# Optimization experiments

Measured on AMD Instinct MI355X. Metric: run time of the kernel, lower is better.

## Reference

```python
import jax, jax.numpy as jnp
import numpy as np

DIM = 384
FRACTION = 16   # quant_bits=16 -> fixed-point fraction bits
INTEGER = 16
WEIGHT_BITS = 5
SHIFT_MIN = -(2 ** (WEIGHT_BITS - 1) - 2)  # -14 (DeepShift shift_range for 5-bit)


def _ste(x, qx):
    # straight-through estimator: forward qx, backward identity
    return x + jax.lax.stop_gradient(qx - x)


def _clampabs(w, mn, mx):
    # clamp |w| into [mn, mx], preserving sign (zeros stay zero)
    return jnp.sign(w) * jnp.clip(jnp.abs(w), mn, mx)


def _round_power_of_2(w):
    # w -> sign(w) * 2^round(log2(|w|))
    shift = jnp.round(jnp.log2(jnp.maximum(jnp.abs(w), 1e-30)))
    return jnp.sign(w) * jnp.exp2(shift)


def _round_to_fixed(x, fraction=FRACTION, integer=INTEGER):
    delta = 2.0 ** (-fraction)
    bound = 2.0 ** (integer - 1)
    return jnp.clip(jnp.floor(x / delta) * delta, -bound, bound - 1)


def setup_inputs() -> dict:
    key = jax.random.key(0)
    k1, k2, k3 = jax.random.split(key, 3)
    x = jax.random.normal(k1, (32, DIM, 56, 56), dtype=jnp.float32)
    weight = jax.random.normal(k2, (DIM, 1, 3, 3), dtype=jnp.float32) * 0.1
    bias = jax.random.normal(k3, (DIM,), dtype=jnp.float32) * 0.01
    return {"x": x, "weight": weight, "bias": bias}


def reference(x, weight, bias):
    # weight: clamp magnitude to [2^-14, 2^0], then round to signed power of two (5-bit shift)
    w = _ste(weight, _clampabs(weight, 2.0 ** SHIFT_MIN, 1.0))
    w = _ste(w, _round_power_of_2(w))
    # activations / bias: 16-bit fixed-point rounding
    xq = _ste(x, _round_to_fixed(x))
    bq = _ste(bias, _round_to_fixed(bias))
    # depthwise 3x3 conv, stride 1, padding 1, groups = DIM
    out = jax.lax.conv_general_dilated(
        xq, w,
        window_strides=(1, 1),
        padding=((1, 1), (1, 1)),
        feature_group_count=DIM,
        dimension_numbers=("NCHW", "OIHW", "NCHW"),
    )
    return out + bq[None, :, None, None]
```

## Files before the change

kernel.cpp:

```cpp
#include <hip/hip_runtime.h>


#define DW_C   384
#define DW_H   56
#define DW_W   56
#define DW_HW  (DW_H * DW_W)
#define DW_HW4 (DW_HW / 4)
#define DW_W4  (DW_W / 4)

__device__ __forceinline__ float qfix(float v) {
    v = floorf(v * 65536.0f) * (1.0f / 65536.0f);
    return fminf(fmaxf(v, -32768.0f), 32767.0f);
}

__global__ __launch_bounds__(256) void peg_shift_dwconv(
    const float* __restrict__ x, const float* __restrict__ wgt,
    const float* __restrict__ bias, float* __restrict__ out)
{
    __shared__ float s[DW_HW];

    const int plane = blockIdx.x;
    const int c = plane % DW_C;
    const float* xp = x + (size_t)plane * DW_HW;
    float* op = out + (size_t)plane * DW_HW;

    const float4* xp4 = (const float4*)xp;
    float4* s4 = (float4*)s;
    for (int i = threadIdx.x; i < DW_HW4; i += 256) {
        float4 v = xp4[i];
        v.x = qfix(v.x); v.y = qfix(v.y); v.z = qfix(v.z); v.w = qfix(v.w);
        s4[i] = v;
    }

    float wq[9];
#pragma unroll
    for (int k = 0; k < 9; ++k) {
        float wv = wgt[c * 9 + k];
        float aw = fabsf(wv);
        float cw = fminf(fmaxf(aw, 6.103515625e-05f ), 1.0f);
        float q  = exp2f(rintf(log2f(cw)));
        wq[k] = (wv > 0.0f) ? q : ((wv < 0.0f) ? -q : 0.0f);
    }
    float bq = qfix(bias[c]);

    __syncthreads();

    for (int iv = threadIdx.x; iv < DW_HW4; iv += 256) {
        int h  = iv / DW_W4;
        int w0 = (iv - h * DW_W4) * 4;
        float a0 = bq, a1 = bq, a2 = bq, a3 = bq;
#pragma unroll
        for (int dh = 0; dh < 3; ++dh) {
            int hh = h + dh - 1;
            if (hh < 0 || hh >= DW_H) continue;
            const float* row = s + hh * DW_W;
            float4 m = *(const float4*)(row + w0);
            float left  = (w0 > 0)        ? row[w0 - 1] : 0.0f;
            float right = (w0 < DW_W - 4) ? row[w0 + 4] : 0.0f;
            float wl = wq[dh * 3 + 0], wm = wq[dh * 3 + 1], wr = wq[dh * 3 + 2];
            a0 += left * wl + m.x * wm + m.y * wr;
            a1 += m.x  * wl + m.y * wm + m.z * wr;
            a2 += m.y  * wl + m.z * wm + m.w * wr;
            a3 += m.z  * wl + m.w * wm + right * wr;
        }
        float4 o; o.x = a0; o.y = a1; o.z = a2; o.w = a3;
        ((float4*)op)[iv] = o;
    }
}

extern "C" void kernel_launch(void* const* d_in, const int* in_sizes, int n_in,
                              void* d_out, int out_size, void* d_ws, size_t ws_size,
                              hipStream_t stream) {
    const float* x = (const float*)d_in[0];
    const float* w = (const float*)d_in[1];
    const float* b = (const float*)d_in[2];
    float* out = (float*)d_out;

    int planes = in_sizes[0] / DW_HW;
    peg_shift_dwconv<<<planes, 256, 0, stream>>>(x, w, b, out);
}
```

Measured before the change: 269.6 us.

## Replace LDS plane staging with register rolling row window and lane shuffles

Each 16-lane group now handles half of one channel plane. Each lane owns a 4-wide column strip and walks 28 rows down the plane, keeping three quantized rows in registers and prefetching the next raw row. Horizontal halo values come from wavefront shuffles instead of shared memory, which removes the LDS fill, the block barrier and the repeated LDS reads. The cost is 2 of every 16 lanes idling (56 columns only need 14 strips) and extra halo row loads at the split between the two halves.

```diff
diff --git a/kernel.cpp b/kernel.cpp
--- a/kernel.cpp
+++ b/kernel.cpp
@@ -5,66 +5,89 @@
 #define DW_H   56
 #define DW_W   56
 #define DW_HW  (DW_H * DW_W)
-#define DW_HW4 (DW_HW / 4)
-#define DW_W4  (DW_W / 4)
+#define HALF_H 28
 
 __device__ __forceinline__ float qfix(float v) {
     v = floorf(v * 65536.0f) * (1.0f / 65536.0f);
     return fminf(fmaxf(v, -32768.0f), 32767.0f);
 }
 
+struct QRow { float l; float4 m; float r; };
+
 __global__ __launch_bounds__(256) void peg_shift_dwconv(
     const float* __restrict__ x, const float* __restrict__ wgt,
     const float* __restrict__ bias, float* __restrict__ out)
 {
-    __shared__ float s[DW_HW];
-
-    const int plane = blockIdx.x;
-    const int c = plane % DW_C;
-    const float* xp = x + (size_t)plane * DW_HW;
-    float* op = out + (size_t)plane * DW_HW;
-
-    const float4* xp4 = (const float4*)xp;
-    float4* s4 = (float4*)s;
-    for (int i = threadIdx.x; i < DW_HW4; i += 256) {
-        float4 v = xp4[i];
-        v.x = qfix(v.x); v.y = qfix(v.y); v.z = qfix(v.z); v.w = qfix(v.w);
-        s4[i] = v;
-    }
+    const int lane16 = threadIdx.x & 15;
+    const int g      = threadIdx.x >> 4;
+    const int unit   = blockIdx.x * 16 + g;
+    const int plane  = unit >> 1;
+    const int half   = unit & 1;
+    const int c      = plane % DW_C;
+    const int strip  = lane16;
+    const bool active = strip < 14;
+    const int w0     = strip * 4;
 
     float wq[9];
 #pragma unroll
     for (int k = 0; k < 9; ++k) {
         float wv = wgt[c * 9 + k];
-        float aw = fabsf(wv);
-        float cw = fminf(fmaxf(aw, 6.103515625e-05f ), 1.0f);
+        float cw = fminf(fmaxf(fabsf(wv), 6.103515625e-05f ), 1.0f);
         float q  = exp2f(rintf(log2f(cw)));
         wq[k] = (wv > 0.0f) ? q : ((wv < 0.0f) ? -q : 0.0f);
     }
-    float bq = qfix(bias[c]);
+    const float bq = qfix(bias[c]);
 
-    __syncthreads();
+    const float* xp = x   + (size_t)plane * DW_HW + w0;
+    float*       op = out + (size_t)plane * DW_HW + w0;
+    const int h0 = half * HALF_H;
 
-    for (int iv = threadIdx.x; iv < DW_HW4; iv += 256) {
-        int h  = iv / DW_W4;
-        int w0 = (iv - h * DW_W4) * 4;
+    auto load_row = [&](int r) -> float4 {
+        if (active && r >= 0 && r < DW_H)
+            return *(const float4*)(xp + r * DW_W);
+        return make_float4(0.f, 0.f, 0.f, 0.f);
+    };
+
+    auto process = [&](float4 raw) -> QRow {
+        QRow t;
+        t.m.x = qfix(raw.x); t.m.y = qfix(raw.y);
+        t.m.z = qfix(raw.z); t.m.w = qfix(raw.w);
+        float up = __shfl_up(t.m.w, 1, 64);
+        float dn = __shfl_down(t.m.x, 1, 64);
+        t.l = (strip > 0)  ? up : 0.f;
+        t.r = (strip < 13) ? dn : 0.f;
+        return t;
+    };
+
+    float4 ra   = load_row(h0 - 1);
+    float4 rb   = load_row(h0);
+    float4 rawc = load_row(h0 + 1);
+    QRow qm1 = process(ra);
+    QRow q0  = process(rb);
+
+    for (int i = 0; i < HALF_H; ++i) {
+        float4 rawn = load_row(h0 + i + 2);
+        QRow q1 = process(rawc);
+
         float a0 = bq, a1 = bq, a2 = bq, a3 = bq;
-#pragma unroll
-        for (int dh = 0; dh < 3; ++dh) {
-            int hh = h + dh - 1;
-            if (hh < 0 || hh >= DW_H) continue;
-            const float* row = s + hh * DW_W;
-            float4 m = *(const float4*)(row + w0);
-            float left  = (w0 > 0)        ? row[w0 - 1] : 0.0f;
-            float right = (w0 < DW_W - 4) ? row[w0 + 4] : 0.0f;
-            float wl = wq[dh * 3 + 0], wm = wq[dh * 3 + 1], wr = wq[dh * 3 + 2];
-            a0 += left * wl + m.x * wm + m.y * wr;
-            a1 += m.x  * wl + m.y * wm + m.z * wr;
-            a2 += m.y  * wl + m.z * wm + m.w * wr;
-            a3 += m.z  * wl + m.w * wm + right * wr;
+        a0 += qm1.l   * wq[0] + qm1.m.x * wq[1] + qm1.m.y * wq[2];
+        a1 += qm1.m.x * wq[0] + qm1.m.y * wq[1] + qm1.m.z * wq[2];
+        a2 += qm1.m.y * wq[0] + qm1.m.z * wq[1] + qm1.m.w * wq[2];
+        a3 += qm1.m.z * wq[0] + qm1.m.w * wq[1] + qm1.r   * wq[2];
+        a0 += q0.l   * wq[3] + q0.m.x * wq[4] + q0.m.y * wq[5];
+        a1 += q0.m.x * wq[3] + q0.m.y * wq[4] + q0.m.z * wq[5];
+        a2 += q0.m.y * wq[3] + q0.m.z * wq[4] + q0.m.w * wq[5];
+        a3 += q0.m.z * wq[3] + q0.m.w * wq[4] + q0.r   * wq[5];
+        a0 += q1.l   * wq[6] + q1.m.x * wq[7] + q1.m.y * wq[8];
+        a1 += q1.m.x * wq[6] + q1.m.y * wq[7] + q1.m.z * wq[8];
+        a2 += q1.m.y * wq[6] + q1.m.z * wq[7] + q1.m.w * wq[8];
+        a3 += q1.m.z * wq[6] + q1.m.w * wq[7] + q1.r   * wq[8];
+
+        if (active) {
+            float4 o; o.x = a0; o.y = a1; o.z = a2; o.w = a3;
+            *(float4*)(op + (h0 + i) * DW_W) = o;
         }
-        float4 o; o.x = a0; o.y = a1; o.z = a2; o.w = a3;
-        ((float4*)op)[iv] = o;
+        qm1 = q0; q0 = q1; rawc = rawn;
     }
 }
 
@@ -77,5 +100,6 @@
     float* out = (float*)d_out;
 
     int planes = in_sizes[0] / DW_HW;
-    peg_shift_dwconv<<<planes, 256, 0, stream>>>(x, w, b, out);
+    int blocks = planes * 2 / 16;
+    peg_shift_dwconv<<<blocks, 256, 0, stream>>>(x, w, b, out);
 }
```

After: 291.1 us. +8.0%, slower.

## Replace LDS staging with per-wave register streaming and shuffle-based halo exchange

Applied to the files above, without the earlier changes.

Each wavefront now handles one whole plane. Lanes are laid out as 4 row-groups by 16 column-vectors, and the plane is streamed in 14 groups of 4 rows with the next loads prefetched into registers. Horizontal and vertical halos move through cross-lane shuffles instead of shared memory, which removes the LDS stage and the block barrier. In exchange it adds many shuffles per output, leaves 2 of every 16 lanes idle, and launches a quarter as many blocks.

```diff
diff --git a/kernel.cpp b/kernel.cpp
--- a/kernel.cpp
+++ b/kernel.cpp
@@ -1,70 +1,119 @@
 #include <hip/hip_runtime.h>
 
 
-#define DW_C   384
-#define DW_H   56
-#define DW_W   56
-#define DW_HW  (DW_H * DW_W)
-#define DW_HW4 (DW_HW / 4)
-#define DW_W4  (DW_W / 4)
+#define DW_C    384
+#define DW_H    56
+#define DW_W    56
+#define DW_HW   (DW_H * DW_W)
+#define NGRP    14
 
 __device__ __forceinline__ float qfix(float v) {
     v = floorf(v * 65536.0f) * (1.0f / 65536.0f);
     return fminf(fmaxf(v, -32768.0f), 32767.0f);
 }
 
+struct P3 { float4 U, M, D; };
+
+__device__ __forceinline__ float4 shfl_up4(float4 v, int d) {
+    float4 r;
+    r.x = __shfl_up(v.x, d, 64); r.y = __shfl_up(v.y, d, 64);
+    r.z = __shfl_up(v.z, d, 64); r.w = __shfl_up(v.w, d, 64);
+    return r;
+}
+__device__ __forceinline__ float4 shfl_dn4(float4 v, int d) {
+    float4 r;
+    r.x = __shfl_down(v.x, d, 64); r.y = __shfl_down(v.y, d, 64);
+    r.z = __shfl_down(v.z, d, 64); r.w = __shfl_down(v.w, d, 64);
+    return r;
+}
+
 __global__ __launch_bounds__(256) void peg_shift_dwconv(
     const float* __restrict__ x, const float* __restrict__ wgt,
     const float* __restrict__ bias, float* __restrict__ out)
 {
-    __shared__ float s[DW_HW];
-
-    const int plane = blockIdx.x;
-    const int c = plane % DW_C;
-    const float* xp = x + (size_t)plane * DW_HW;
-    float* op = out + (size_t)plane * DW_HW;
-
-    const float4* xp4 = (const float4*)xp;
-    float4* s4 = (float4*)s;
-    for (int i = threadIdx.x; i < DW_HW4; i += 256) {
-        float4 v = xp4[i];
-        v.x = qfix(v.x); v.y = qfix(v.y); v.z = qfix(v.z); v.w = qfix(v.w);
-        s4[i] = v;
-    }
+    const int lane  = threadIdx.x & 63;
+    const int wave  = threadIdx.x >> 6;
+    const int plane = blockIdx.x * 4 + wave;
+    const int rg    = lane >> 4;
+    const int w4    = lane & 15;
+    const bool active = w4 < 14;
+    const int c     = plane % DW_C;
 
     float wq[9];
 #pragma unroll
     for (int k = 0; k < 9; ++k) {
         float wv = wgt[c * 9 + k];
-        float aw = fabsf(wv);
-        float cw = fminf(fmaxf(aw, 6.103515625e-05f ), 1.0f);
+        float cw = fminf(fmaxf(fabsf(wv), 6.103515625e-05f ), 1.0f);
         float q  = exp2f(rintf(log2f(cw)));
         wq[k] = (wv > 0.0f) ? q : ((wv < 0.0f) ? -q : 0.0f);
     }
-    float bq = qfix(bias[c]);
+    const float bq = qfix(bias[c]);
 
-    __syncthreads();
+    const int   lane_off = rg * DW_W + w4 * 4;
+    const float* xp = x   + (size_t)plane * DW_HW + lane_off;
+    float*       op = out + (size_t)plane * DW_HW + lane_off;
 
-    for (int iv = threadIdx.x; iv < DW_HW4; iv += 256) {
-        int h  = iv / DW_W4;
-        int w0 = (iv - h * DW_W4) * 4;
-        float a0 = bq, a1 = bq, a2 = bq, a3 = bq;
-#pragma unroll
-        for (int dh = 0; dh < 3; ++dh) {
-            int hh = h + dh - 1;
-            if (hh < 0 || hh >= DW_H) continue;
-            const float* row = s + hh * DW_W;
-            float4 m = *(const float4*)(row + w0);
-            float left  = (w0 > 0)        ? row[w0 - 1] : 0.0f;
-            float right = (w0 < DW_W - 4) ? row[w0 + 4] : 0.0f;
-            float wl = wq[dh * 3 + 0], wm = wq[dh * 3 + 1], wr = wq[dh * 3 + 2];
-            a0 += left * wl + m.x * wm + m.y * wr;
-            a1 += m.x  * wl + m.y * wm + m.z * wr;
-            a2 += m.y  * wl + m.z * wm + m.w * wr;
-            a3 += m.z  * wl + m.w * wm + right * wr;
+    auto load_grp = [&](int g) -> float4 {
+        if (active) return *(const float4*)(xp + g * (4 * DW_W));
+        return make_float4(0.f, 0.f, 0.f, 0.f);
+    };
+
+    auto partials = [&](float4 raw) -> P3 {
+        float4 m;
+        m.x = qfix(raw.x); m.y = qfix(raw.y);
+        m.z = qfix(raw.z); m.w = qfix(raw.w);
+        float l = __shfl_up(m.w, 1, 64);   l = (w4 > 0)  ? l : 0.f;
+        float r = __shfl_down(m.x, 1, 64); r = (w4 < 13) ? r : 0.f;
+        P3 p;
+        p.U.x = l*wq[0] + m.x*wq[1] + m.y*wq[2];
+        p.U.y = m.x*wq[0] + m.y*wq[1] + m.z*wq[2];
+        p.U.z = m.y*wq[0] + m.z*wq[1] + m.w*wq[2];
+        p.U.w = m.z*wq[0] + m.w*wq[1] + r*wq[2];
+        p.M.x = bq + l*wq[3] + m.x*wq[4] + m.y*wq[5];
+        p.M.y = bq + m.x*wq[3] + m.y*wq[4] + m.z*wq[5];
+        p.M.z = bq + m.y*wq[3] + m.z*wq[4] + m.w*wq[5];
+        p.M.w = bq + m.z*wq[3] + m.w*wq[4] + r*wq[5];
+        p.D.x = l*wq[6] + m.x*wq[7] + m.y*wq[8];
+        p.D.y = m.x*wq[6] + m.y*wq[7] + m.z*wq[8];
+        p.D.z = m.y*wq[6] + m.z*wq[7] + m.w*wq[8];
+        p.D.w = m.z*wq[6] + m.w*wq[7] + r*wq[8];
+        return p;
+    };
+
+    float4 raw0 = load_grp(0);
+    float4 rawN = load_grp(1);
+    P3 P0 = partials(raw0);
+    float4 carryU = make_float4(0.f, 0.f, 0.f, 0.f);
+    const float4 zero4 = make_float4(0.f, 0.f, 0.f, 0.f);
+
+    for (int i = 0; i < NGRP; ++i) {
+        float4 raw2 = (i + 2 < NGRP) ? load_grp(i + 2) : zero4;
+
+        P3 P1;
+        if (i + 1 < NGRP) P1 = partials(rawN);
+        else              { P1.U = zero4; P1.M = zero4; P1.D = zero4; }
+
+        float4 dn_cross = shfl_up4(P1.D, 48);
+        float4 upS = shfl_up4(P0.U, 16);
+        float4 dnS = shfl_dn4(P0.D, 16);
+        float4 up, dn;
+        up.x = (rg > 0) ? upS.x : carryU.x;  up.y = (rg > 0) ? upS.y : carryU.y;
+        up.z = (rg > 0) ? upS.z : carryU.z;  up.w = (rg > 0) ? upS.w : carryU.w;
+        dn.x = (rg < 3) ? dnS.x : dn_cross.x; dn.y = (rg < 3) ? dnS.y : dn_cross.y;
+        dn.z = (rg < 3) ? dnS.z : dn_cross.z; dn.w = (rg < 3) ? dnS.w : dn_cross.w;
+
+        if (active) {
+            float4 o;
+            o.x = up.x + P0.M.x + dn.x;
+            o.y = up.y + P0.M.y + dn.y;
+            o.z = up.z + P0.M.z + dn.z;
+            o.w = up.w + P0.M.w + dn.w;
+            *(float4*)(op + i * (4 * DW_W)) = o;
         }
-        float4 o; o.x = a0; o.y = a1; o.z = a2; o.w = a3;
-        ((float4*)op)[iv] = o;
+
+        carryU = shfl_dn4(P0.U, 48);
+        P0 = P1;
+        rawN = raw2;
     }
 }
 
@@ -77,5 +126,6 @@
     float* out = (float*)d_out;
 
     int planes = in_sizes[0] / DW_HW;
-    peg_shift_dwconv<<<planes, 256, 0, stream>>>(x, w, b, out);
+    int blocks = planes / 4;
+    peg_shift_dwconv<<<blocks, 256, 0, stream>>>(x, w, b, out);
 }
```

Measured after the change: 275.1 us. 2.0% more time.
